# Kernel tuning notes

Measured on AMD Instinct MI355X. Metric: run time of the kernel, lower is better.

## Reference

```python
import jax, jax.numpy as jnp
import numpy as np

NUM_HEADS = 16
NUM_HIDDENS = 1024
D_K = NUM_HIDDENS // NUM_HEADS
NEG_INF = -1.0e9


def setup_inputs() -> dict:
    key = jax.random.key(0)
    kx, kq, kk, kv, ko, kl = jax.random.split(key, 6)
    B, S, D = 2, 2048, NUM_HIDDENS
    scale = 1.0 / np.sqrt(D)
    return {
        "X": jax.random.normal(kx, (B, S, D), dtype=jnp.float32),
        "valid_lens": jax.random.randint(kl, (B,), 0, S, dtype=jnp.int64),
        "W_q": jax.random.normal(kq, (D, D), dtype=jnp.float32) * scale,
        "W_k": jax.random.normal(kk, (D, D), dtype=jnp.float32) * scale,
        "W_v": jax.random.normal(kv, (D, D), dtype=jnp.float32) * scale,
        "W_o": jax.random.normal(ko, (D, D), dtype=jnp.float32) * scale,
    }


def _split_heads(x):
    # [B, S, D] -> [B, H, S, d_k]
    B, S, _ = x.shape
    return x.reshape(B, S, NUM_HEADS, D_K).transpose(0, 2, 1, 3)


def reference(X, valid_lens, W_q, W_k, W_v, W_o):
    B, S, D = X.shape
    # nn.Linear(bias=False): y = x @ W.T  (W is [out, in])
    Q = _split_heads(jnp.einsum("bsd,ed->bse", X, W_q))  # [B,H,S,dk]
    K = _split_heads(jnp.einsum("bsd,ed->bse", X, W_k))
    V = _split_heads(jnp.einsum("bsd,ed->bse", X, W_v))

    scores = jnp.einsum("bhqd,bhkd->bhqk", Q, K) / jnp.sqrt(
        jnp.asarray(D_K, dtype=X.dtype)
    )  # [B,H,S,S]

    # key-position mask per batch: positions >= valid_len get -1e9
    mask = jnp.arange(S)[None, :] >= valid_lens[:, None]  # [B,S]
    scores = jnp.where(mask[:, None, None, :], jnp.asarray(NEG_INF, X.dtype), scores)

    attn = jax.nn.softmax(scores, axis=-1)  # dropout p=0 -> identity
    out = jnp.einsum("bhqk,bhkd->bhqd", attn, V)  # [B,H,S,dk]
    out = out.transpose(0, 2, 1, 3).reshape(B, S, D)
    return jnp.einsum("bsd,ed->bse", out, W_o)
```

## Files before the change

kernel.cpp:

```cpp
#include <hip/hip_runtime.h>
#include <stdint.h>

#define S_LEN 2048
#define BATCH 2
#define DMODEL 1024
#define NHEAD 16
#define DK 64
#define MROWS (BATCH * S_LEN)

typedef __attribute__((ext_vector_type(8))) short bf16x8;
typedef __attribute__((ext_vector_type(4))) float f32x4;
typedef __attribute__((ext_vector_type(16))) float f32x16;
typedef __attribute__((ext_vector_type(4))) short short4v;

#define VMCNT(N) asm volatile("s_waitcnt vmcnt(" #N ")" ::: "memory")

__device__ __forceinline__ short f2b(float f) {
    union { float f; uint32_t u; } c; c.f = f;
    uint32_t u = c.u;
    return (short)((u + 0x7fffu + ((u >> 16) & 1u)) >> 16);
}

__device__ __forceinline__ void gload16(const void* g, void* l) {
    __builtin_amdgcn_global_load_lds(
        (const __attribute__((address_space(1))) void*)g,
        (__attribute__((address_space(3))) void*)l, 16, 0, 0);
}

__global__ void cvt_kernel(const float* __restrict__ X, const float* __restrict__ Wq,
                           const float* __restrict__ Wk, const float* __restrict__ Wv,
                           const float* __restrict__ Wo,
                           short* __restrict__ Xb, short* __restrict__ Wqb,
                           short* __restrict__ Wkb, short* __restrict__ Wvb,
                           short* __restrict__ Wob) {
    const float* src; short* dst; int n4;
    switch (blockIdx.y) {
        case 0:  src = X;  dst = Xb;  n4 = MROWS * DMODEL / 4;  break;
        case 1:  src = Wq; dst = Wqb; n4 = DMODEL * DMODEL / 4; break;
        case 2:  src = Wk; dst = Wkb; n4 = DMODEL * DMODEL / 4; break;
        case 3:  src = Wv; dst = Wvb; n4 = DMODEL * DMODEL / 4; break;
        default: src = Wo; dst = Wob; n4 = DMODEL * DMODEL / 4; break;
    }
    for (int i = blockIdx.x * blockDim.x + threadIdx.x; i < n4;
         i += gridDim.x * blockDim.x) {
        float4 v = ((const float4*)src)[i];
        short4v o;
        o[0] = f2b(v.x); o[1] = f2b(v.y); o[2] = f2b(v.z); o[3] = f2b(v.w);
        ((short4v*)dst)[i] = o;
    }
}

template <int OUT_F32>
__global__ __launch_bounds__(256) void gemm_bt(
    const short* __restrict__ A,
    const short* __restrict__ Bt0, const short* __restrict__ Bt1,
    const short* __restrict__ Bt2,
    short* __restrict__ Cb0, short* __restrict__ Cb1, short* __restrict__ Cb2,
    float* __restrict__ Cf, const int* __restrict__ vlens, int M, int N, int K) {
    __shared__ short sA[3][128 * 32];
    __shared__ short sB[3][128 * 32];

    const short* Bt = Bt0;
    short* Cb = Cb0;
    if (blockIdx.z == 1) { Bt = Bt1; Cb = Cb1; }
    else if (blockIdx.z == 2) { Bt = Bt2; Cb = Cb2; }

    const int brow = blockIdx.y * 128;
    if (!OUT_F32 && blockIdx.z >= 1 && vlens) {
        int vlb = vlens[brow >> 11];
        if (vlb <= 0 || vlb > S_LEN) vlb = S_LEN;
        else vlb = (vlb + 63) & ~63;
        if ((brow & (S_LEN - 1)) >= vlb) return;
    }

    const int tid = threadIdx.x;
    const int lane = tid & 63;
    const int wid = tid >> 6;
    const int wr = wid >> 1, wc = wid & 1;
    const int bcol = blockIdx.x * 128;
    const int lr = lane & 15;
    const int kh = (lane >> 4) << 3;
    const int swg = ((lr >> 1) & 3) << 3;
    const int khs = kh ^ swg;

    f32x4 acc[4][4] = {};

    const int idx0 = tid, idx1 = tid + 256;
    const int ar0 = idx0 >> 2, ak0 = ((idx0 & 3) << 3) ^ (((ar0 >> 1) & 3) << 3);
    const int ar1 = idx1 >> 2, ak1 = ((idx1 & 3) << 3) ^ (((ar1 >> 1) & 3) << 3);

    const short* gA0 = A + (size_t)(brow + ar0) * K + ak0;
    const short* gA1 = A + (size_t)(brow + ar1) * K + ak1;
    const short* gB0 = Bt + (size_t)(bcol + ar0) * K + ak0;
    const short* gB1 = Bt + (size_t)(bcol + ar1) * K + ak1;

#define G_STAGE(KT, PA, PB)                                   \
    do {                                                      \
        const int k0_ = (KT) << 5;                            \
        gload16(gA0 + k0_, (PA) + idx0 * 8);                  \
        gload16(gA1 + k0_, (PA) + idx1 * 8);                  \
        gload16(gB0 + k0_, (PB) + idx0 * 8);                  \
        gload16(gB1 + k0_, (PB) + idx1 * 8);                  \
    } while (0)

    const int nk = K >> 5;
    short* pA0 = &sA[0][0]; short* pA1 = &sA[1][0]; short* pA2 = &sA[2][0];
    short* pB0 = &sB[0][0]; short* pB1 = &sB[1][0]; short* pB2 = &sB[2][0];

    G_STAGE(0, pA0, pB0);
    G_STAGE(1, pA1, pB1);

    for (int kt = 0; kt < nk; ++kt) {
        if (kt == nk - 1) { VMCNT(0); } else { VMCNT(4); }
        __builtin_amdgcn_s_barrier();
        if (kt + 2 < nk) G_STAGE(kt + 2, pA2, pB2);

        bf16x8 a[4], b[4];
#pragma unroll
        for (int mt = 0; mt < 4; ++mt)
            a[mt] = *(const bf16x8*)&pA0[(wr * 64 + mt * 16 + lr) * 32 + khs];
#pragma unroll
        for (int nt = 0; nt < 4; ++nt)
            b[nt] = *(const bf16x8*)&pB0[(wc * 64 + nt * 16 + lr) * 32 + khs];
        __builtin_amdgcn_s_setprio(1);
#pragma unroll
        for (int mt = 0; mt < 4; ++mt)
#pragma unroll
            for (int nt = 0; nt < 4; ++nt)
                acc[mt][nt] = __builtin_amdgcn_mfma_f32_16x16x32_bf16(
                    a[mt], b[nt], acc[mt][nt], 0, 0, 0);
        __builtin_amdgcn_s_setprio(0);

        short* tA = pA0; pA0 = pA1; pA1 = pA2; pA2 = tA;
        short* tB = pB0; pB0 = pB1; pB1 = pB2; pB2 = tB;
    }
#undef G_STAGE

    const int rbase = (lane >> 4) << 2;
    const bool vtrans = (!OUT_F32) && (blockIdx.z == 2);
#pragma unroll
    for (int mt = 0; mt < 4; ++mt) {
#pragma unroll
        for (int nt = 0; nt < 4; ++nt) {
            if (vtrans) {
                int row0 = brow + wr * 64 + mt * 16 + rbase;
                int col = bcol + wc * 64 + nt * 16 + lr;
                int bb = row0 >> 11, key = row0 & 2047;
                int hh = col >> 6, d = col & 63;
                short4v pk;
#pragma unroll
                for (int j = 0; j < 4; ++j) pk[j] = f2b(acc[mt][nt][j]);
                *(short4v*)&Cb[((size_t)((bb * 16 + hh) * 64 + d)) * S_LEN + key] = pk;
            } else {
#pragma unroll
                for (int j = 0; j < 4; ++j) {
                    int row = brow + wr * 64 + mt * 16 + rbase + j;
                    int col = bcol + wc * 64 + nt * 16 + lr;
                    if (OUT_F32)
                        Cf[(size_t)row * N + col] = acc[mt][nt][j];
                    else
                        Cb[(size_t)row * N + col] = f2b(acc[mt][nt][j]);
                }
            }
        }
    }
}

__global__ __launch_bounds__(256, 2) void attn_kernel(
    const short* __restrict__ Q, const short* __restrict__ K,
    const short* __restrict__ Vt, short* __restrict__ O,
    const int* __restrict__ vlens) {
    __shared__ short sK[5][64 * 64];
    __shared__ short sV[5][64 * 64];

    const int tid = threadIdx.x;
    const int lane = tid & 63;
    const int w = tid >> 6;
    const int id = blockIdx.x;
    const int xcd = id & 7;
    const int r = id >> 3;
    const int b = (r >> 5) & 1;
    const int h = (xcd << 1) | (r & 1);
    const int qb = (r >> 1) & 15;
    const int rl_ = lane & 31;
    const int g = lane >> 5;

    int vl = vlens[b];
    if (vl < 0) vl = 0;
    if (vl > S_LEN) vl = S_LEN;
    const bool allm = (vl == 0);
    if (allm) vl = S_LEN;
    const int nT = (vl + 63) >> 6;
    const int nFull = ((vl & 63) == 0) ? nT : nT - 1;

    const size_t rowbase = (size_t)(b * S_LEN) * DMODEL + h * DK;
    const short* vt = Vt + ((size_t)((b * 16 + h) * 64)) * S_LEN;

    const int q = qb * 128 + w * 32 + rl_;
    const short* qA = Q + rowbase + (size_t)q * DMODEL;
    bf16x8 qf[4];
#pragma unroll
    for (int f = 0; f < 4; ++f)
        qf[f] = *(const bf16x8*)(qA + f * 16 + g * 8);
    if (allm) {
#pragma unroll
        for (int f = 0; f < 4; ++f)
#pragma unroll
            for (int i = 0; i < 8; ++i) qf[f][i] = 0;
    }

    f32x16 oac0 = {}, oac1 = {};
    float m_run = -1e30f, mc = -1e30f, l_run = 0.f;
    const float CEXP = 0.18033688011112042f;
    const float THRADD = 44.361419556f;

    const int rsw = (((rl_ & 7) ^ ((rl_ >> 3) & 3)) << 3);
    int lofs[4];
#pragma unroll
    for (int f = 0; f < 4; ++f)
        lofs[f] = rl_ * 64 + ((f * 16 + g * 8) ^ rsw);

    const int kr = tid >> 3;
    const int kc = (((tid & 7) ^ (kr & 7) ^ ((kr >> 3) & 3)) << 3);
    const short* kBase = K + rowbase + (size_t)kr * DMODEL + kc;
    const short* vBase = vt + (size_t)kr * S_LEN + kc;

    short* const sK0 = &sK[0][0];
    short* const sV0 = &sV[0][0];
#define KBUF(i) (sK0 + (i) * 4096)
#define VBUF(i) (sV0 + (i) * 4096)

#define A_STAGE(T, PK, PV)                                                      \
    do {                                                                        \
        const short* kg_ = kBase + (size_t)((T) * 64) * DMODEL;                 \
        gload16(kg_, (PK) + tid * 8);                                           \
        gload16(kg_ + (size_t)32 * DMODEL, (PK) + (tid + 256) * 8);             \
        const short* vg_ = vBase + (T) * 64;                                    \
        gload16(vg_, (PV) + tid * 8);                                           \
        gload16(vg_ + (size_t)32 * S_LEN, (PV) + (tid + 256) * 8);              \
    } while (0)

#define MK_FRAG(A0, A1, A2, A3)                                                 \
    ({ union { uint32_t u[4]; bf16x8 v; } _f;                                   \
       _f.u[0] = (A0); _f.u[1] = (A1); _f.u[2] = (A2); _f.u[3] = (A3); _f.v; })

    bf16x8 pF0 = {}, pF1 = {}, pF2 = {}, pF3 = {};

#define PV_BODY(PV)                                                             \
    do {                                                                        \
        bf16x8 v0 = *(const bf16x8*)&(PV)[lofs[0]];                             \
        bf16x8 v1 = *(const bf16x8*)&(PV)[lofs[0] + 2048];                      \
        oac0 = __builtin_amdgcn_mfma_f32_32x32x16_bf16(v0, pF0, oac0, 0, 0, 0); \
        oac1 = __builtin_amdgcn_mfma_f32_32x32x16_bf16(v1, pF0, oac1, 0, 0, 0); \
        v0 = *(const bf16x8*)&(PV)[lofs[1]];                                    \
        v1 = *(const bf16x8*)&(PV)[lofs[1] + 2048];                             \
        oac0 = __builtin_amdgcn_mfma_f32_32x32x16_bf16(v0, pF1, oac0, 0, 0, 0); \
        oac1 = __builtin_amdgcn_mfma_f32_32x32x16_bf16(v1, pF1, oac1, 0, 0, 0); \
        v0 = *(const bf16x8*)&(PV)[lofs[2]];                                    \
        v1 = *(const bf16x8*)&(PV)[lofs[2] + 2048];                             \
        oac0 = __builtin_amdgcn_mfma_f32_32x32x16_bf16(v0, pF2, oac0, 0, 0, 0); \
        oac1 = __builtin_amdgcn_mfma_f32_32x32x16_bf16(v1, pF2, oac1, 0, 0, 0); \
        v0 = *(const bf16x8*)&(PV)[lofs[3]];                                    \
        v1 = *(const bf16x8*)&(PV)[lofs[3] + 2048];                             \
        oac0 = __builtin_amdgcn_mfma_f32_32x32x16_bf16(v0, pF3, oac0, 0, 0, 0); \
        oac1 = __builtin_amdgcn_mfma_f32_32x32x16_bf16(v1, pF3, oac1, 0, 0, 0); \
    } while (0)

#define SM_BODY(MASKED_C)                                                       \
    do {                                                                        \
        constexpr bool MASKED = MASKED_C;                                       \
        if (MASKED) {                                                           \
            _Pragma("unroll")                                                   \
            for (int rg = 0; rg < 16; ++rg) {                                   \
                int key0 = t * 64 + (rg & 3) + 8 * (rg >> 2) + 4 * g;           \
                if (key0 >= vl) s0[rg] = -3.0e38f;                              \
                if (key0 + 32 >= vl) s1[rg] = -3.0e38f;                         \
            }                                                                   \
        }                                                                       \
        float x0 = fmaxf(fmaxf(s0[0], s0[1]), fmaxf(s0[2], s0[3]));             \
        float x1 = fmaxf(fmaxf(s0[4], s0[5]), fmaxf(s0[6], s0[7]));             \
        float x2 = fmaxf(fmaxf(s0[8], s0[9]), fmaxf(s0[10], s0[11]));           \
        float x3 = fmaxf(fmaxf(s0[12], s0[13]), fmaxf(s0[14], s0[15]));         \
        float x4 = fmaxf(fmaxf(s1[0], s1[1]), fmaxf(s1[2], s1[3]));             \
        float x5 = fmaxf(fmaxf(s1[4], s1[5]), fmaxf(s1[6], s1[7]));             \
        float x6 = fmaxf(fmaxf(s1[8], s1[9]), fmaxf(s1[10], s1[11]));           \
        float x7 = fmaxf(fmaxf(s1[12], s1[13]), fmaxf(s1[14], s1[15]));         \
        float px = fmaxf(fmaxf(fmaxf(x0, x1), fmaxf(x2, x3)),                   \
                         fmaxf(fmaxf(x4, x5), fmaxf(x6, x7)));                  \
        if (__any(px > m_run + THRADD)) {                                       \
            float mx = fmaxf(px, __shfl_xor(px, 32));                           \
            mx = fmaxf(mx, m_run);                                              \
            float scl = __builtin_exp2f((m_run - mx) * CEXP);                   \
            m_run = mx; mc = mx * CEXP;                                         \
            l_run *= scl;                                                       \
            _Pragma("unroll")                                                   \
            for (int i = 0; i < 16; ++i) { oac0[i] *= scl; oac1[i] *= scl; }    \
        }                                                                       \
        uint32_t P0[8], P1[8];                                                  \
        float ls = 0.f;                                                         \
        _Pragma("unroll")                                                       \
        for (int i = 0; i < 8; ++i) {                                           \
            float a0 = __builtin_exp2f(__builtin_fmaf(s0[2 * i], CEXP, -mc));   \
            float a1 = __builtin_exp2f(__builtin_fmaf(s0[2 * i + 1], CEXP, -mc)); \
            float b0 = __builtin_exp2f(__builtin_fmaf(s1[2 * i], CEXP, -mc));   \
            float b1 = __builtin_exp2f(__builtin_fmaf(s1[2 * i + 1], CEXP, -mc)); \
            ls += (a0 + a1) + (b0 + b1);                                        \
            asm("v_cvt_pk_bf16_f32 %0, %1, %2" : "=v"(P0[i]) : "v"(a0), "v"(a1)); \
            asm("v_cvt_pk_bf16_f32 %0, %1, %2" : "=v"(P1[i]) : "v"(b0), "v"(b1)); \
        }                                                                       \
        l_run += ls;                                                            \
        asm volatile("v_permlane32_swap_b32 %0, %1" : "+v"(P0[0]), "+v"(P0[2])); \
        asm volatile("v_permlane32_swap_b32 %0, %1" : "+v"(P0[1]), "+v"(P0[3])); \
        asm volatile("v_permlane32_swap_b32 %0, %1" : "+v"(P0[4]), "+v"(P0[6])); \
        asm volatile("v_permlane32_swap_b32 %0, %1" : "+v"(P0[5]), "+v"(P0[7])); \
        asm volatile("v_permlane32_swap_b32 %0, %1" : "+v"(P1[0]), "+v"(P1[2])); \
        asm volatile("v_permlane32_swap_b32 %0, %1" : "+v"(P1[1]), "+v"(P1[3])); \
        asm volatile("v_permlane32_swap_b32 %0, %1" : "+v"(P1[4]), "+v"(P1[6])); \
        asm volatile("v_permlane32_swap_b32 %0, %1" : "+v"(P1[5]), "+v"(P1[7])); \
        pF0 = MK_FRAG(P0[0], P0[1], P0[2], P0[3]);                              \
        pF1 = MK_FRAG(P0[4], P0[5], P0[6], P0[7]);                              \
        pF2 = MK_FRAG(P1[0], P1[1], P1[2], P1[3]);                              \
        pF3 = MK_FRAG(P1[4], P1[5], P1[6], P1[7]);                              \
    } while (0)

    A_STAGE(0, KBUF(0), VBUF(0));
    if (nT > 1) A_STAGE(1, KBUF(1), VBUF(1));
    if (nT > 2) A_STAGE(2, KBUF(2), VBUF(2));

    int cur = 0, stg = 3, prv = 4;
    for (int t = 0; t < nT; ++t) {
        const int rem = nT - 1 - t;
        if (rem >= 2) { VMCNT(8); }
        else if (rem == 1) { VMCNT(4); }
        else { VMCNT(0); }
        __builtin_amdgcn_s_barrier();
        if (t + 3 < nT) A_STAGE(t + 3, KBUF(stg), VBUF(stg));

        const short* PK = KBUF(cur);
        f32x16 s0 = {}, s1 = {};
        __builtin_amdgcn_s_setprio(1);
#pragma unroll
        for (int f = 0; f < 4; ++f) {
            bf16x8 ka = *(const bf16x8*)&PK[lofs[f]];
            bf16x8 kb2 = *(const bf16x8*)&PK[lofs[f] + 2048];
            s0 = __builtin_amdgcn_mfma_f32_32x32x16_bf16(ka, qf[f], s0, 0, 0, 0);
            s1 = __builtin_amdgcn_mfma_f32_32x32x16_bf16(kb2, qf[f], s1, 0, 0, 0);
        }
        if (t > 0) PV_BODY(VBUF(prv));
        __builtin_amdgcn_s_setprio(0);

        if (t < nFull) SM_BODY(false);
        else SM_BODY(true);

        prv = cur;
        cur = (cur == 4) ? 0 : cur + 1;
        stg = (stg == 4) ? 0 : stg + 1;
    }
    __builtin_amdgcn_s_setprio(1);
    PV_BODY(VBUF(prv));
    __builtin_amdgcn_s_setprio(0);

#undef SM_BODY
#undef PV_BODY
#undef A_STAGE
#undef MK_FRAG
#undef KBUF
#undef VBUF

    float lt = l_run + __shfl_xor(l_run, 32);
    float rl2 = 1.f / lt;

    short* orow = O + rowbase + (size_t)q * DMODEL;
#pragma unroll
    for (int r2 = 0; r2 < 4; ++r2) {
        short4v pk0, pk1;
#pragma unroll
        for (int j = 0; j < 4; ++j) {
            pk0[j] = f2b(oac0[r2 * 4 + j] * rl2);
            pk1[j] = f2b(oac1[r2 * 4 + j] * rl2);
        }
        int d0 = r2 * 8 + 4 * g;
        *(short4v*)&orow[d0] = pk0;
        *(short4v*)&orow[32 + d0] = pk1;
    }
}

extern "C" void kernel_launch(void* const* d_in, const int* in_sizes, int n_in,
                              void* d_out, int out_size, void* d_ws, size_t ws_size,
                              hipStream_t stream) {
    const float* X = (const float*)d_in[0];
    const int* vlens = (const int*)d_in[1];
    const float* Wq = (const float*)d_in[2];
    const float* Wk = (const float*)d_in[3];
    const float* Wv = (const float*)d_in[4];
    const float* Wo = (const float*)d_in[5];
    float* out = (float*)d_out;

    short* Xb = (short*)d_ws;
    short* Wqb = Xb + (size_t)MROWS * DMODEL;
    short* Wkb = Wqb + (size_t)DMODEL * DMODEL;
    short* Wvb = Wkb + (size_t)DMODEL * DMODEL;
    short* Wob = Wvb + (size_t)DMODEL * DMODEL;
    short* Qb = Wob + (size_t)DMODEL * DMODEL;
    short* Kb = Qb + (size_t)MROWS * DMODEL;
    short* Vtb = Kb + (size_t)MROWS * DMODEL;
    short* Ob = Vtb + (size_t)MROWS * DMODEL;

    cvt_kernel<<<dim3(512, 5), 256, 0, stream>>>(X, Wq, Wk, Wv, Wo, Xb, Wqb, Wkb,
                                                 Wvb, Wob);
    gemm_bt<0><<<dim3(8, 32, 3), 256, 0, stream>>>(Xb, Wqb, Wkb, Wvb, Qb, Kb, Vtb,
                                                   nullptr, vlens, MROWS, DMODEL,
                                                   DMODEL);
    attn_kernel<<<dim3(512), 256, 0, stream>>>(Qb, Kb, Vtb, Ob, vlens);
    gemm_bt<1><<<dim3(8, 32, 1), 256, 0, stream>>>(Ob, Wob, Wob, Wob, nullptr,
                                                   nullptr, nullptr, out, nullptr,
                                                   MROWS, DMODEL, DMODEL);
}
```

Before: 101.9 us.

## Fuse K and V projections into one GEMM sharing the X tile

```diff
diff --git a/kernel.cpp b/kernel.cpp
--- a/kernel.cpp
+++ b/kernel.cpp
@@ -47,6 +47,145 @@
         short4v o;
         o[0] = f2b(v.x); o[1] = f2b(v.y); o[2] = f2b(v.z); o[3] = f2b(v.w);
         ((short4v*)dst)[i] = o;
+    }
+}
+
+__global__ __launch_bounds__(256) void gemm_qkv(
+    const short* __restrict__ A,
+    const short* __restrict__ Wq, const short* __restrict__ Wk,
+    const short* __restrict__ Wv,
+    short* __restrict__ Qo, short* __restrict__ Ko, short* __restrict__ Vto,
+    const int* __restrict__ vlens) {
+    __shared__ short sA[3][128 * 32];
+    __shared__ short sB1[3][128 * 32];
+    __shared__ short sB2[3][128 * 32];
+
+    const int Kd = DMODEL, N = DMODEL;
+    const bool fused = (blockIdx.z == 1);
+    const int brow = blockIdx.y * 128;
+    if (fused) {
+        int vlb = vlens[brow >> 11];
+        if (vlb <= 0 || vlb > S_LEN) vlb = S_LEN;
+        else vlb = (vlb + 63) & ~63;
+        if ((brow & (S_LEN - 1)) >= vlb) return;
+    }
+
+    const int tid = threadIdx.x;
+    const int lane = tid & 63;
+    const int wid = tid >> 6;
+    const int wr = wid >> 1, wc = wid & 1;
+    const int bcol = blockIdx.x * 128;
+    const int lr = lane & 15;
+    const int kh = (lane >> 4) << 3;
+    const int swg = ((lr >> 1) & 3) << 3;
+    const int khs = kh ^ swg;
+
+    f32x4 acc1[4][4] = {};
+    f32x4 acc2[4][4] = {};
+
+    const int idx0 = tid, idx1 = tid + 256;
+    const int ar0 = idx0 >> 2, ak0 = ((idx0 & 3) << 3) ^ (((ar0 >> 1) & 3) << 3);
+    const int ar1 = idx1 >> 2, ak1 = ((idx1 & 3) << 3) ^ (((ar1 >> 1) & 3) << 3);
+
+    const short* Bt1 = fused ? Wk : Wq;
+    const short* gA0 = A + (size_t)(brow + ar0) * Kd + ak0;
+    const short* gA1 = A + (size_t)(brow + ar1) * Kd + ak1;
+    const short* gB10 = Bt1 + (size_t)(bcol + ar0) * Kd + ak0;
+    const short* gB11 = Bt1 + (size_t)(bcol + ar1) * Kd + ak1;
+    const short* gB20 = Wv + (size_t)(bcol + ar0) * Kd + ak0;
+    const short* gB21 = Wv + (size_t)(bcol + ar1) * Kd + ak1;
+
+#define Q_STAGE(KT, PA, PB1, PB2)                              \
+    do {                                                       \
+        const int k0_ = (KT) << 5;                             \
+        gload16(gA0 + k0_, (PA) + idx0 * 8);                   \
+        gload16(gA1 + k0_, (PA) + idx1 * 8);                   \
+        gload16(gB10 + k0_, (PB1) + idx0 * 8);                 \
+        gload16(gB11 + k0_, (PB1) + idx1 * 8);                 \
+        if (fused) {                                           \
+            gload16(gB20 + k0_, (PB2) + idx0 * 8);             \
+            gload16(gB21 + k0_, (PB2) + idx1 * 8);             \
+        }                                                      \
+    } while (0)
+
+    const int nk = Kd >> 5;
+    short* pA0 = &sA[0][0];  short* pA1 = &sA[1][0];  short* pA2 = &sA[2][0];
+    short* pB10 = &sB1[0][0]; short* pB11 = &sB1[1][0]; short* pB12 = &sB1[2][0];
+    short* pB20 = &sB2[0][0]; short* pB21 = &sB2[1][0]; short* pB22 = &sB2[2][0];
+
+    Q_STAGE(0, pA0, pB10, pB20);
+    Q_STAGE(1, pA1, pB11, pB21);
+
+    for (int kt = 0; kt < nk; ++kt) {
+        if (kt == nk - 1) { VMCNT(0); }
+        else if (fused) { VMCNT(6); }
+        else { VMCNT(4); }
+        __builtin_amdgcn_s_barrier();
+        if (kt + 2 < nk) Q_STAGE(kt + 2, pA2, pB12, pB22);
+
+        bf16x8 a[4];
+#pragma unroll
+        for (int mt = 0; mt < 4; ++mt)
+            a[mt] = *(const bf16x8*)&pA0[(wr * 64 + mt * 16 + lr) * 32 + khs];
+        {
+            bf16x8 b[4];
+#pragma unroll
+            for (int nt = 0; nt < 4; ++nt)
+                b[nt] = *(const bf16x8*)&pB10[(wc * 64 + nt * 16 + lr) * 32 + khs];
+            __builtin_amdgcn_s_setprio(1);
+#pragma unroll
+            for (int mt = 0; mt < 4; ++mt)
+#pragma unroll
+                for (int nt = 0; nt < 4; ++nt)
+                    acc1[mt][nt] = __builtin_amdgcn_mfma_f32_16x16x32_bf16(
+                        a[mt], b[nt], acc1[mt][nt], 0, 0, 0);
+            __builtin_amdgcn_s_setprio(0);
+        }
+        if (fused) {
+            bf16x8 b[4];
+#pragma unroll
+            for (int nt = 0; nt < 4; ++nt)
+                b[nt] = *(const bf16x8*)&pB20[(wc * 64 + nt * 16 + lr) * 32 + khs];
+            __builtin_amdgcn_s_setprio(1);
+#pragma unroll
+            for (int mt = 0; mt < 4; ++mt)
+#pragma unroll
+                for (int nt = 0; nt < 4; ++nt)
+                    acc2[mt][nt] = __builtin_amdgcn_mfma_f32_16x16x32_bf16(
+                        a[mt], b[nt], acc2[mt][nt], 0, 0, 0);
+            __builtin_amdgcn_s_setprio(0);
+        }
+
+        short* t;
+        t = pA0;  pA0 = pA1;  pA1 = pA2;  pA2 = t;
+        t = pB10; pB10 = pB11; pB11 = pB12; pB12 = t;
+        t = pB20; pB20 = pB21; pB21 = pB22; pB22 = t;
+    }
+#undef Q_STAGE
+
+    const int rbase = (lane >> 4) << 2;
+    short* C1 = fused ? Ko : Qo;
+#pragma unroll
+    for (int mt = 0; mt < 4; ++mt) {
+#pragma unroll
+        for (int nt = 0; nt < 4; ++nt) {
+#pragma unroll
+            for (int j = 0; j < 4; ++j) {
+                int row = brow + wr * 64 + mt * 16 + rbase + j;
+                int col = bcol + wc * 64 + nt * 16 + lr;
+                C1[(size_t)row * N + col] = f2b(acc1[mt][nt][j]);
+            }
+            if (fused) {
+                int row0 = brow + wr * 64 + mt * 16 + rbase;
+                int col = bcol + wc * 64 + nt * 16 + lr;
+                int bb = row0 >> 11, key = row0 & 2047;
+                int hh = col >> 6, d = col & 63;
+                short4v pk;
+#pragma unroll
+                for (int j = 0; j < 4; ++j) pk[j] = f2b(acc2[mt][nt][j]);
+                *(short4v*)&Vto[((size_t)((bb * 16 + hh) * 64 + d)) * S_LEN + key] = pk;
+            }
+        }
     }
 }
 
@@ -408,9 +547,8 @@
 
     cvt_kernel<<<dim3(512, 5), 256, 0, stream>>>(X, Wq, Wk, Wv, Wo, Xb, Wqb, Wkb,
                                                  Wvb, Wob);
-    gemm_bt<0><<<dim3(8, 32, 3), 256, 0, stream>>>(Xb, Wqb, Wkb, Wvb, Qb, Kb, Vtb,
-                                                   nullptr, vlens, MROWS, DMODEL,
-                                                   DMODEL);
+    gemm_qkv<<<dim3(8, 32, 2), 256, 0, stream>>>(Xb, Wqb, Wkb, Wvb, Qb, Kb, Vtb,
+                                                 vlens);
     attn_kernel<<<dim3(512), 256, 0, stream>>>(Qb, Kb, Vtb, Ob, vlens);
     gemm_bt<1><<<dim3(8, 32, 1), 256, 0, stream>>>(Ob, Wob, Wob, Wob, nullptr,
                                                    nullptr, nullptr, out, nullptr,
```

Measured after the change: 106.3 us. +4.3%, slower.
